# Kernel optimization log

Hardware: AMD Instinct MI355X
Metric: run time of the kernel (lower is better)

The kernel has to match this reference:

```python
import jax, jax.numpy as jnp
import numpy as np

B_, C_, T_, F_ = 1, 64, 256, 128
D_CONV, D_STATE, DT_RANK = 4, 16, 4
D_INNER = 2 * C_
EPS = 1e-5


def setup_inputs():
    key = jax.random.key(0)
    ks = jax.random.split(key, 12)
    s = 0.05
    return {
        'x': jax.random.normal(ks[0], (B_, C_, T_, F_), jnp.float32),
        'norm_w': jnp.ones((4, C_), jnp.float32),
        'in_proj_w': jax.random.normal(ks[1], (4, 2 * D_INNER, C_), jnp.float32) * s,
        'conv_w': jax.random.normal(ks[2], (4, D_INNER, 1, D_CONV), jnp.float32) * 0.3,
        'conv_b': jnp.zeros((4, D_INNER), jnp.float32),
        'x_proj_w': jax.random.normal(ks[3], (4, DT_RANK + 2 * D_STATE, D_INNER), jnp.float32) * s,
        'dt_proj_w': jax.random.normal(ks[4], (4, D_INNER, DT_RANK), jnp.float32) * 0.1,
        'dt_proj_b': jnp.log(jnp.expm1(jax.random.uniform(ks[5], (4, D_INNER), jnp.float32, 1e-3, 0.1))),
        'A_log': jnp.log(jax.random.uniform(ks[6], (4, D_INNER, D_STATE), jnp.float32, 0.5, 16.0)),
        'Dp': jnp.ones((4, D_INNER), jnp.float32),
        'out_proj_w': jax.random.normal(ks[7], (4, C_, D_INNER), jnp.float32) * s,
        'tlin_w': jax.random.normal(ks[8], (2 * C_, C_), jnp.float32) * s,
        'tlin_b': jnp.zeros((C_,), jnp.float32),
        'flin_w': jax.random.normal(ks[9], (2 * C_, C_), jnp.float32) * s,
        'flin_b': jnp.zeros((C_,), jnp.float32),
    }


def _rmsnorm(x, w):
    return x * jax.lax.rsqrt(jnp.mean(x * x, axis=-1, keepdims=True) + EPS) * w


def _mamba(u, p):
    # u: (N, L, d_model) ; selective-scan Mamba mixer
    N, L, _ = u.shape
    xz = jnp.einsum('nld,ed->nle', u, p['in_proj_w'])  # (N,L,2*di)
    x, z = jnp.split(xz, 2, axis=-1)
    # causal depthwise conv over time
    xT = jnp.swapaxes(x, 1, 2)  # (N, di, L)
    xc = jax.lax.conv_general_dilated(xT, p['conv_w'], (1,), [(D_CONV - 1, 0)],
                                      feature_group_count=D_INNER)
    x = jnp.swapaxes(jax.nn.silu(xc + p['conv_b'][None, :, None]), 1, 2)  # (N,L,di)
    xdbl = jnp.einsum('nld,ed->nle', x, p['x_proj_w'])
    dt, Bm, Cm = jnp.split(xdbl, [DT_RANK, DT_RANK + D_STATE], axis=-1)
    dt = jax.nn.softplus(jnp.einsum('nlr,dr->nld', dt, p['dt_proj_w']) + p['dt_proj_b'])
    A = -jnp.exp(p['A_log'])  # (di, ds)

    def step(h, inp):
        dt_t, B_t, C_t, x_t = inp  # (N,di),(N,ds),(N,ds),(N,di)
        dA = jnp.exp(dt_t[:, :, None] * A)  # (N,di,ds)
        h = dA * h + dt_t[:, :, None] * B_t[:, None, :] * x_t[:, :, None]
        return h, jnp.einsum('nds,ns->nd', h, C_t)

    h0 = jnp.zeros((N, D_INNER, D_STATE), u.dtype)
    _, ys = jax.lax.scan(step, h0, (jnp.swapaxes(dt, 0, 1), jnp.swapaxes(Bm, 0, 1),
                                    jnp.swapaxes(Cm, 0, 1), jnp.swapaxes(x, 0, 1)))
    y = jnp.swapaxes(ys, 0, 1) + x * p['Dp']
    y = y * jax.nn.silu(z)
    return jnp.einsum('nld,od->nlo', y, p['out_proj_w'])


def _block(u, p):
    # mamba Block with residual: out = mixer(rmsnorm(u)) + u
    return _mamba(_rmsnorm(u, p['norm_w']), p) + u


def _bimamba(u, pf, pb):
    yf = _block(u, pf)
    yb = jnp.flip(_block(jnp.flip(u, 1), pb), 1)
    return jnp.concatenate([yf, yb], axis=-1)


def _pick(i, norm_w, in_proj_w, conv_w, conv_b, x_proj_w, dt_proj_w, dt_proj_b, A_log, Dp, out_proj_w):
    return dict(norm_w=norm_w[i], in_proj_w=in_proj_w[i], conv_w=conv_w[i], conv_b=conv_b[i],
                x_proj_w=x_proj_w[i], dt_proj_w=dt_proj_w[i], dt_proj_b=dt_proj_b[i],
                A_log=A_log[i], Dp=Dp[i], out_proj_w=out_proj_w[i])


def _tfmamba(x, norm_w, in_proj_w, conv_w, conv_b, x_proj_w, dt_proj_w, dt_proj_b,
             A_log, Dp, out_proj_w, tlin_w, tlin_b, flin_w, flin_b):
    b, c, t, f = x.shape
    P = [_pick(i, norm_w, in_proj_w, conv_w, conv_b, x_proj_w, dt_proj_w, dt_proj_b, A_log, Dp, out_proj_w)
         for i in range(4)]
    # time axis
    xt = jnp.reshape(jnp.transpose(x, (0, 3, 2, 1)), (b * f, t, c))
    xt_out = _bimamba(xt, P[0], P[1])  # (b*f, t, 2c)
    xt = xt + jnp.einsum('nti,io->nto', xt_out, tlin_w) + tlin_b
    # frequency axis
    xf = jnp.reshape(jnp.transpose(jnp.reshape(xt, (b, f, t, c)), (0, 2, 1, 3)), (b * t, f, c))
    xf_out = _bimamba(xf, P[2], P[3])  # (b*t, f, 2c)
    xf = xf + jnp.einsum('nfi,io->nfo', xf_out, flin_w) + flin_b
    return jnp.transpose(jnp.reshape(xf, (b, t, f, c)), (0, 3, 1, 2))


def reference(x, norm_w, in_proj_w, conv_w, conv_b, x_proj_w, dt_proj_w, dt_proj_b,
              A_log, Dp, out_proj_w, tlin_w, tlin_b, flin_w, flin_b):
    return _tfmamba(x, norm_w, in_proj_w, conv_w, conv_b, x_proj_w, dt_proj_w, dt_proj_b,
                    A_log, Dp, out_proj_w, tlin_w, tlin_b, flin_w, flin_b)
```

## Files before the change

kernel.cpp:

```cpp
#include <hip/hip_runtime.h>
#include <math.h>

#define C_DIM 64
#define T_DIM 256
#define F_DIM 128
#define DI    128
#define DS    16
#define CK    16

typedef __attribute__((ext_vector_type(8))) short bf16x8;
typedef __attribute__((ext_vector_type(4))) float f32x4;

__device__ __forceinline__ float silu_f(float v){ return v / (1.0f + __expf(-v)); }

__device__ __forceinline__ unsigned short f2bf(float f){
  union{float f; unsigned u;} v; v.f = f;
  unsigned r = v.u + 0x7FFFu + ((v.u >> 16) & 1u);
  return (unsigned short)(r >> 16);
}

__global__ __launch_bounds__(256) void k_prep(const float* __restrict__ ipw,
                                              const float* __restrict__ opw,
                                              const float* __restrict__ xpw,
                                              const float* __restrict__ tlw,
                                              unsigned short* __restrict__ wbuf){
  const int i = blockIdx.x*256 + threadIdx.x;
  if(i < 65536){
    wbuf[i] = f2bf(ipw[i]);
  } else if(i < 98304){
    wbuf[i] = f2bf(opw[i - 65536]);
  } else if(i < 122880){
    const int j = i - 98304;
    const int p = j / 6144, rr = (j - p*6144) >> 7, k = j & 127;
    wbuf[i] = (rr < 36) ? f2bf(xpw[p*4608 + rr*128 + k]) : (unsigned short)0;
  } else {
    const int j = i - 122880;
    const int o = j >> 7, k = j & 127;
    wbuf[i] = f2bf(tlw[k*64 + o]);
  }
}

__global__ __launch_bounds__(256) void k_transpose_in(const float* __restrict__ x,
                                                      float* __restrict__ xt){
  __shared__ float tile[64][133];
  const int t = blockIdx.x;
  {
    const int fi = threadIdx.x & 127, cg = threadIdx.x >> 7;
    for(int c = cg*32; c < cg*32 + 32; ++c)
      tile[c][fi] = x[(size_t)c*32768 + (size_t)t*128 + fi];
  }
  __syncthreads();
  {
    const int ci = threadIdx.x & 63, fg = threadIdx.x >> 6;
    for(int f = fg*32; f < fg*32 + 32; ++f)
      xt[(size_t)f*16384 + (size_t)t*64 + ci] = tile[ci][f];
  }
}

__global__ __launch_bounds__(256, 2) void k_mamba(
    const float* __restrict__ src, int N, int L, long long sn, long long sl,
    int pbase,
    const float* __restrict__ norm_w,   const unsigned short* __restrict__ wbf,
    const float* __restrict__ conv_w,   const float* __restrict__ conv_b,
    const float* __restrict__ dt_proj_w,
    const float* __restrict__ dt_proj_b,const float* __restrict__ A_log,
    const float* __restrict__ Dp,       float* __restrict__ obuf)
{
  __shared__ __align__(16) unsigned short u_bf[CK][64];
  __shared__ float x_s[CK+3][132];
  __shared__ float z_s[CK][132];
  __shared__ float xc_s[CK][132];
  __shared__ __align__(16) unsigned short xc_bf[CK][128];
  __shared__ float dt_s[CK][132];
  __shared__ float dtr_s[CK][4];
  __shared__ float B_s[CK][20];
  __shared__ float C_s[CK][20];
  __shared__ __align__(16) unsigned short y_bf[CK][128];
  __shared__ float y_out[CK][68];
  __shared__ float w_cv[512];
  __shared__ float b_cv[128];
  __shared__ float w_dt[512];
  __shared__ float b_dt[128];
  __shared__ float dvec[128];
  __shared__ float nw[64];

  const int tid = threadIdx.x;
  const int bid = blockIdx.x;
  const int dir = (bid >= N) ? 1 : 0;
  const int n   = dir ? (bid - N) : bid;
  const int p   = pbase + dir;

  const int lane = tid & 63;
  const int wv   = tid >> 6;
  const int fr   = lane & 15;
  const int fk   = (lane >> 4) << 3;

  for(int i = tid; i < 512; i += 256){ w_cv[i] = conv_w[p*512 + i]; w_dt[i] = dt_proj_w[p*512 + i]; }
  if(tid < 128){ b_cv[tid] = conv_b[p*128 + tid]; b_dt[tid] = dt_proj_b[p*128 + tid]; dvec[tid] = Dp[p*128 + tid]; }
  if(tid < 64) nw[tid] = norm_w[p*64 + tid];
  for(int i = tid; i < 3*128; i += 256){ x_s[i >> 7][i & 127] = 0.0f; }

  const unsigned short* WinB  = wbf + (size_t)p*16384;
  const unsigned short* WoutB = wbf + 65536 + (size_t)p*8192;
  const unsigned short* XpB   = wbf + 98304 + (size_t)p*6144;
  bf16x8 aW[4][2];
  #pragma unroll
  for(int ot = 0; ot < 4; ++ot)
    #pragma unroll
    for(int kh = 0; kh < 2; ++kh)
      aW[ot][kh] = *(const bf16x8*)(WinB + (wv*64 + ot*16 + fr)*64 + kh*32 + fk);
  bf16x8 aO[4];
  #pragma unroll
  for(int kc = 0; kc < 4; ++kc)
    aO[kc] = *(const bf16x8*)(WoutB + (wv*16 + fr)*128 + kc*32 + fk);
  bf16x8 aXP[4];
  if(wv < 3){
    #pragma unroll
    for(int kc = 0; kc < 4; ++kc)
      aXP[kc] = *(const bf16x8*)(XpB + (wv*16 + fr)*128 + kc*32 + fk);
  }

  const int d_own = tid >> 1;
  const int sh    = (tid & 1) * 8;
  float A_r[8], h[8];
  #pragma unroll
  for(int i = 0; i < 8; ++i){
    A_r[i] = -__expf(A_log[p*2048 + d_own*16 + sh + i]) * 1.44269504f;
    h[i] = 0.0f;
  }
  __syncthreads();

  for(int c0 = 0; c0 < L; c0 += CK){
    if(c0 > 0){
      for(int i = tid; i < 3*128; i += 256){
        int r = i >> 7, ch = i & 127;
        x_s[r][ch] = x_s[CK + r][ch];
      }
    }
    {
      const int g = tid >> 4, j = tid & 15, c4 = j*4;
      const int l = c0 + g;
      const int lo = dir ? (L - 1 - l) : l;
      const float4 v = *(const float4*)(src + (size_t)n*sn + (size_t)lo*sl + c4);
      float ssq = v.x*v.x + v.y*v.y + v.z*v.z + v.w*v.w;
      ssq += __shfl_xor(ssq, 1); ssq += __shfl_xor(ssq, 2);
      ssq += __shfl_xor(ssq, 4); ssq += __shfl_xor(ssq, 8);
      const float sc = rsqrtf(ssq * (1.0f/64.0f) + 1e-5f);
      ushort4 pk;
      pk.x = f2bf(v.x * sc * nw[c4+0]);
      pk.y = f2bf(v.y * sc * nw[c4+1]);
      pk.z = f2bf(v.z * sc * nw[c4+2]);
      pk.w = f2bf(v.w * sc * nw[c4+3]);
      *(ushort4*)&u_bf[g][c4] = pk;
    }
    __syncthreads();

    {
      const bf16x8 b0 = *(const bf16x8*)&u_bf[fr][fk];
      const bf16x8 b1 = *(const bf16x8*)&u_bf[fr][32 + fk];
      #pragma unroll
      for(int ot = 0; ot < 4; ++ot){
        f32x4 acc = {0.f, 0.f, 0.f, 0.f};
        acc = __builtin_amdgcn_mfma_f32_16x16x32_bf16(aW[ot][0], b0, acc, 0, 0, 0);
        acc = __builtin_amdgcn_mfma_f32_16x16x32_bf16(aW[ot][1], b1, acc, 0, 0, 0);
        const int ob = wv*64 + ot*16 + ((lane >> 4) << 2);
        if(wv < 2){
          #pragma unroll
          for(int r = 0; r < 4; ++r) x_s[3 + fr][ob + r] = acc[r];
        } else {
          #pragma unroll
          for(int r = 0; r < 4; ++r) z_s[fr][ob + r - 128] = acc[r];
        }
      }
    }
    __syncthreads();

    {
      const int g = tid >> 4, j = tid & 15;
      #pragma unroll
      for(int i = 0; i < 8; ++i){
        const int ch = j + 16*i;
        float a = b_cv[ch];
        a += w_cv[ch*4+0] * x_s[g+0][ch];
        a += w_cv[ch*4+1] * x_s[g+1][ch];
        a += w_cv[ch*4+2] * x_s[g+2][ch];
        a += w_cv[ch*4+3] * x_s[g+3][ch];
        const float s = silu_f(a);
        xc_s[g][ch]  = s;
        xc_bf[g][ch] = f2bf(s);
      }
    }
    __syncthreads();

    if(wv < 3){
      f32x4 acc = {0.f, 0.f, 0.f, 0.f};
      #pragma unroll
      for(int kc = 0; kc < 4; ++kc){
        const bf16x8 b = *(const bf16x8*)&xc_bf[fr][kc*32 + fk];
        acc = __builtin_amdgcn_mfma_f32_16x16x32_bf16(aXP[kc], b, acc, 0, 0, 0);
      }
      const int ob36 = wv*16 + ((lane >> 4) << 2);
      #pragma unroll
      for(int r = 0; r < 4; ++r){
        const int o36 = ob36 + r;
        const float v = acc[r];
        if(o36 < 4)       dtr_s[fr][o36] = v;
        else if(o36 < 20) B_s[fr][o36 - 4] = v;
        else if(o36 < 36) C_s[fr][o36 - 20] = v;
      }
    }
    __syncthreads();

    {
      const int g = tid >> 4, j = tid & 15;
      const float r0 = dtr_s[g][0], r1 = dtr_s[g][1], r2 = dtr_s[g][2], r3 = dtr_s[g][3];
      #pragma unroll
      for(int i = 0; i < 8; ++i){
        const int d = j + 16*i;
        float a = b_dt[d] + w_dt[d*4+0]*r0 + w_dt[d*4+1]*r1 + w_dt[d*4+2]*r2 + w_dt[d*4+3]*r3;
        dt_s[g][d] = fmaxf(a, 0.0f) + log1pf(__expf(-fabsf(a)));
      }
    }
    __syncthreads();

    for(int l = 0; l < CK; ++l){
      const float dtv = dt_s[l][d_own];
      const float xv  = xc_s[l][d_own];
      const float4 b0 = *(const float4*)&B_s[l][sh];
      const float4 b1 = *(const float4*)&B_s[l][sh + 4];
      const float4 g0 = *(const float4*)&C_s[l][sh];
      const float4 g1 = *(const float4*)&C_s[l][sh + 4];
      const float bb[8] = {b0.x,b0.y,b0.z,b0.w,b1.x,b1.y,b1.z,b1.w};
      const float cc[8] = {g0.x,g0.y,g0.z,g0.w,g1.x,g1.y,g1.z,g1.w};
      const float dx = dtv * xv;
      float yp = 0.0f;
      #pragma unroll
      for(int i = 0; i < 8; ++i){
        h[i] = exp2f(dtv * A_r[i]) * h[i] + dx * bb[i];
        yp += h[i] * cc[i];
      }
      const float yo = yp + __shfl_xor(yp, 1);
      if((tid & 1) == 0) xc_s[l][d_own] = yo + xv * dvec[d_own];
    }
    __syncthreads();

    {
      const int g = tid >> 4, j = tid & 15;
      #pragma unroll
      for(int i = 0; i < 8; ++i){
        const int ch = j + 16*i;
        y_bf[g][ch] = f2bf(xc_s[g][ch] * silu_f(z_s[g][ch]));
      }
    }
    __syncthreads();

    {
      f32x4 acc = {0.f, 0.f, 0.f, 0.f};
      #pragma unroll
      for(int kc = 0; kc < 4; ++kc){
        const bf16x8 b = *(const bf16x8*)&y_bf[fr][kc*32 + fk];
        acc = __builtin_amdgcn_mfma_f32_16x16x32_bf16(aO[kc], b, acc, 0, 0, 0);
      }
      const int o2 = wv*16 + ((lane >> 4) << 2);
      #pragma unroll
      for(int r = 0; r < 4; ++r) y_out[fr][o2 + r] = acc[r];
    }
    __syncthreads();

    {
      const int o = tid & 63, lg = tid >> 6;
      #pragma unroll
      for(int li = 0; li < 4; ++li){
        const int l = c0 + lg*4 + li;
        const int lo = dir ? (L - 1 - l) : l;
        obuf[((size_t)dir*32768 + (size_t)n*L + lo)*64 + o] = y_out[lg*4 + li][o];
      }
    }
  }
}

__global__ __launch_bounds__(256) void k_comb_time(
    const float* __restrict__ xt, const float* __restrict__ obuf,
    const unsigned short* __restrict__ wbf, const float* __restrict__ tlin_b,
    float* __restrict__ xt2)
{
  __shared__ __align__(16) unsigned short in_bf[64][128];
  __shared__ float xs[64][72];
  const int tid = threadIdx.x;
  const int lane = tid & 63, wv = tid >> 6;
  const int fr = lane & 15, fk = (lane >> 4) << 3;
  const int tk0 = blockIdx.x*64;

  const unsigned short* TL = wbf + 122880;
  bf16x8 aT[4];
  #pragma unroll
  for(int kc = 0; kc < 4; ++kc)
    aT[kc] = *(const bf16x8*)(TL + (wv*16 + fr)*128 + kc*32 + fk);

  {
    const int tg = tid >> 2, q = tid & 3;
    #pragma unroll
    for(int s = 0; s < 4; ++s){
      const int c4 = q*16 + s*4;
      const float4 xv = *(const float4*)(xt   + ((size_t)tk0 + tg)*64 + c4);
      const float4 fv = *(const float4*)(obuf + ((size_t)tk0 + tg)*64 + c4);
      const float4 bv = *(const float4*)(obuf + ((size_t)32768 + tk0 + tg)*64 + c4);
      ushort4 pf, pb;
      pf.x = f2bf(fv.x + xv.x); pf.y = f2bf(fv.y + xv.y);
      pf.z = f2bf(fv.z + xv.z); pf.w = f2bf(fv.w + xv.w);
      pb.x = f2bf(bv.x + xv.x); pb.y = f2bf(bv.y + xv.y);
      pb.z = f2bf(bv.z + xv.z); pb.w = f2bf(bv.w + xv.w);
      *(ushort4*)&in_bf[tg][c4]      = pf;
      *(ushort4*)&in_bf[tg][64 + c4] = pb;
      *(float4*)&xs[tg][c4] = xv;
    }
  }
  __syncthreads();

  {
    const int ob = wv*16 + ((lane >> 4) << 2);
    const float4 tb = *(const float4*)(tlin_b + ob);
    const float tbr[4] = {tb.x, tb.y, tb.z, tb.w};
    #pragma unroll
    for(int tt = 0; tt < 4; ++tt){
      f32x4 acc = {0.f, 0.f, 0.f, 0.f};
      #pragma unroll
      for(int kc = 0; kc < 4; ++kc){
        const bf16x8 b = *(const bf16x8*)&in_bf[tt*16 + fr][kc*32 + fk];
        acc = __builtin_amdgcn_mfma_f32_16x16x32_bf16(aT[kc], b, acc, 0, 0, 0);
      }
      const int token = tt*16 + fr;
      #pragma unroll
      for(int r = 0; r < 4; ++r)
        xs[token][ob + r] += tbr[r] + acc[r];
    }
  }
  __syncthreads();

  {
    const int tg = tid >> 2, q = tid & 3;
    #pragma unroll
    for(int s = 0; s < 4; ++s){
      const int c4 = q*16 + s*4;
      *(float4*)(xt2 + ((size_t)tk0 + tg)*64 + c4) = *(const float4*)&xs[tg][c4];
    }
  }
}

__global__ __launch_bounds__(256) void k_final(
    const float* __restrict__ xt2, const float* __restrict__ obuf,
    const float* __restrict__ flin_w, const float* __restrict__ flin_b,
    float* __restrict__ out)
{
  __shared__ float res_s[128][68];
  const int t = blockIdx.x, tid = threadIdx.x;
  const int f = tid >> 1, half = tid & 1, cbase = half*32;

  const float4* xr = (const float4*)(xt2  + (size_t)f*16384 + (size_t)t*64);
  const float4* fr = (const float4*)(obuf + ((size_t)t*128 + f)*64);
  const float4* br = (const float4*)(obuf + ((size_t)32768 + (size_t)t*128 + f)*64);

  float res[32];
  {
    const float4* fb = (const float4*)(flin_b + cbase);
    #pragma unroll
    for(int q = 0; q < 8; ++q){
      const float4 xv = xr[(cbase >> 2) + q], b = fb[q];
      res[q*4+0] = xv.x + b.x; res[q*4+1] = xv.y + b.y;
      res[q*4+2] = xv.z + b.z; res[q*4+3] = xv.w + b.w;
    }
  }
  for(int i4 = 0; i4 < 16; ++i4){
    const float4 xv4 = xr[i4], of4 = fr[i4], ob4 = br[i4];
    const float af[4] = {of4.x + xv4.x, of4.y + xv4.y, of4.z + xv4.z, of4.w + xv4.w};
    const float ab[4] = {ob4.x + xv4.x, ob4.y + xv4.y, ob4.z + xv4.z, ob4.w + xv4.w};
    #pragma unroll
    for(int ii = 0; ii < 4; ++ii){
      const int i = i4*4 + ii;
      const float4* F0 = (const float4*)(flin_w + i*64 + cbase);
      const float4* F1 = (const float4*)(flin_w + (64 + i)*64 + cbase);
      #pragma unroll
      for(int q = 0; q < 8; ++q){
        const float4 w0 = F0[q], w1 = F1[q];
        res[q*4+0] += af[ii]*w0.x + ab[ii]*w1.x;
        res[q*4+1] += af[ii]*w0.y + ab[ii]*w1.y;
        res[q*4+2] += af[ii]*w0.z + ab[ii]*w1.z;
        res[q*4+3] += af[ii]*w0.w + ab[ii]*w1.w;
      }
    }
  }
  #pragma unroll
  for(int c = 0; c < 32; ++c) res_s[f][cbase + c] = res[c];
  __syncthreads();
  {
    const int fi = tid & 127, cq = tid >> 7;
    for(int c = cq*32; c < cq*32 + 32; ++c)
      out[(size_t)c*32768 + (size_t)t*128 + fi] = res_s[fi][c];
  }
}

extern "C" void kernel_launch(void* const* d_in, const int* in_sizes, int n_in,
                              void* d_out, int out_size, void* d_ws, size_t ws_size,
                              hipStream_t stream){
  (void)in_sizes; (void)n_in; (void)out_size; (void)ws_size;
  const float* x         = (const float*)d_in[0];
  const float* norm_w    = (const float*)d_in[1];
  const float* in_proj_w = (const float*)d_in[2];
  const float* conv_w    = (const float*)d_in[3];
  const float* conv_b    = (const float*)d_in[4];
  const float* x_proj_w  = (const float*)d_in[5];
  const float* dt_proj_w = (const float*)d_in[6];
  const float* dt_proj_b = (const float*)d_in[7];
  const float* A_log     = (const float*)d_in[8];
  const float* Dp        = (const float*)d_in[9];
  const float* out_proj_w= (const float*)d_in[10];
  const float* tlin_w    = (const float*)d_in[11];
  const float* tlin_b    = (const float*)d_in[12];
  const float* flin_w    = (const float*)d_in[13];
  const float* flin_b    = (const float*)d_in[14];
  float* out = (float*)d_out;

  float* xt_buf = (float*)d_ws;
  float* obuf   = xt_buf + (size_t)(1u << 21);
  float* xt2    = obuf   + (size_t)(1u << 22);

  unsigned short* wbf = (unsigned short*)d_out;

  hipLaunchKernelGGL(k_prep, dim3(512), dim3(256), 0, stream,
      in_proj_w, out_proj_w, x_proj_w, tlin_w, wbf);

  hipLaunchKernelGGL(k_transpose_in, dim3(256), dim3(256), 0, stream, x, xt_buf);

  hipLaunchKernelGGL(k_mamba, dim3(256), dim3(256), 0, stream,
      xt_buf, 128, 256, (long long)16384, (long long)64, 0,
      norm_w, wbf, conv_w, conv_b, dt_proj_w, dt_proj_b,
      A_log, Dp, obuf);

  hipLaunchKernelGGL(k_comb_time, dim3(512), dim3(256), 0, stream,
      xt_buf, obuf, wbf, tlin_b, xt2);

  hipLaunchKernelGGL(k_mamba, dim3(512), dim3(256), 0, stream,
      xt2, 256, 128, (long long)64, (long long)16384, 2,
      norm_w, wbf, conv_w, conv_b, dt_proj_w, dt_proj_b,
      A_log, Dp, obuf);

  hipLaunchKernelGGL(k_final, dim3(256), dim3(256), 0, stream,
      xt2, obuf, flin_w, flin_b, out);
}
```

Baseline: 431.3 us.

## Fuse dt softplus and gating into scan, swizzle LDS, store output directly

Result: slower. 447.6 us (+3.8%).

```diff
diff --git a/kernel.cpp b/kernel.cpp
--- a/kernel.cpp
+++ b/kernel.cpp
@@ -17,6 +17,13 @@
   union{float f; unsigned u;} v; v.f = f;
   unsigned r = v.u + 0x7FFFu + ((v.u >> 16) & 1u);
   return (unsigned short)(r >> 16);
+}
+
+__device__ __forceinline__ int swz64(int row, int col){
+  return row*64 + (col ^ ((row & 7) << 3));
+}
+__device__ __forceinline__ int swz128(int row, int col){
+  return row*128 + (col ^ ((row & 7) << 3));
 }
 
 __global__ __launch_bounds__(256) void k_prep(const float* __restrict__ ipw,
@@ -57,7 +64,7 @@
   }
 }
 
-__global__ __launch_bounds__(256, 2) void k_mamba(
+__global__ __launch_bounds__(256, 3) void k_mamba(
     const float* __restrict__ src, int N, int L, long long sn, long long sl,
     int pbase,
     const float* __restrict__ norm_w,   const unsigned short* __restrict__ wbf,
@@ -66,22 +73,17 @@
     const float* __restrict__ dt_proj_b,const float* __restrict__ A_log,
     const float* __restrict__ Dp,       float* __restrict__ obuf)
 {
-  __shared__ __align__(16) unsigned short u_bf[CK][64];
+  __shared__ __align__(16) unsigned short u_bf[CK*64];
   __shared__ float x_s[CK+3][132];
   __shared__ float z_s[CK][132];
   __shared__ float xc_s[CK][132];
-  __shared__ __align__(16) unsigned short xc_bf[CK][128];
-  __shared__ float dt_s[CK][132];
-  __shared__ float dtr_s[CK][4];
-  __shared__ float B_s[CK][20];
-  __shared__ float C_s[CK][20];
-  __shared__ __align__(16) unsigned short y_bf[CK][128];
-  __shared__ float y_out[CK][68];
+  __shared__ __align__(16) unsigned short xc_bf[CK*128];
+  __shared__ __align__(16) float dtr_s[CK][4];
+  __shared__ __align__(16) float B_s[CK][20];
+  __shared__ __align__(16) float C_s[CK][20];
+  __shared__ __align__(16) unsigned short y_bf[CK*128];
   __shared__ float w_cv[512];
   __shared__ float b_cv[128];
-  __shared__ float w_dt[512];
-  __shared__ float b_dt[128];
-  __shared__ float dvec[128];
   __shared__ float nw[64];
 
   const int tid = threadIdx.x;
@@ -95,8 +97,8 @@
   const int fr   = lane & 15;
   const int fk   = (lane >> 4) << 3;
 
-  for(int i = tid; i < 512; i += 256){ w_cv[i] = conv_w[p*512 + i]; w_dt[i] = dt_proj_w[p*512 + i]; }
-  if(tid < 128){ b_cv[tid] = conv_b[p*128 + tid]; b_dt[tid] = dt_proj_b[p*128 + tid]; dvec[tid] = Dp[p*128 + tid]; }
+  for(int i = tid; i < 512; i += 256) w_cv[i] = conv_w[p*512 + i];
+  if(tid < 128) b_cv[tid] = conv_b[p*128 + tid];
   if(tid < 64) nw[tid] = norm_w[p*64 + tid];
   for(int i = tid; i < 3*128; i += 256){ x_s[i >> 7][i & 127] = 0.0f; }
 
@@ -122,6 +124,10 @@
 
   const int d_own = tid >> 1;
   const int sh    = (tid & 1) * 8;
+  const int odd   = tid & 1;
+  const float4 wdt4  = *(const float4*)(dt_proj_w + p*512 + d_own*4);
+  const float  bdt_r = dt_proj_b[p*128 + d_own];
+  const float  dvec_r= Dp[p*128 + d_own];
   float A_r[8], h[8];
   #pragma unroll
   for(int i = 0; i < 8; ++i){
@@ -151,13 +157,13 @@
       pk.y = f2bf(v.y * sc * nw[c4+1]);
       pk.z = f2bf(v.z * sc * nw[c4+2]);
       pk.w = f2bf(v.w * sc * nw[c4+3]);
-      *(ushort4*)&u_bf[g][c4] = pk;
+      *(ushort4*)&u_bf[swz64(g, c4)] = pk;
     }
     __syncthreads();
 
     {
-      const bf16x8 b0 = *(const bf16x8*)&u_bf[fr][fk];
-      const bf16x8 b1 = *(const bf16x8*)&u_bf[fr][32 + fk];
+      const bf16x8 b0 = *(const bf16x8*)&u_bf[swz64(fr, fk)];
+      const bf16x8 b1 = *(const bf16x8*)&u_bf[swz64(fr, 32 + fk)];
       #pragma unroll
       for(int ot = 0; ot < 4; ++ot){
         f32x4 acc = {0.f, 0.f, 0.f, 0.f};
@@ -186,8 +192,8 @@
         a += w_cv[ch*4+2] * x_s[g+2][ch];
         a += w_cv[ch*4+3] * x_s[g+3][ch];
         const float s = silu_f(a);
-        xc_s[g][ch]  = s;
-        xc_bf[g][ch] = f2bf(s);
+        xc_s[g][ch] = s;
+        xc_bf[swz128(g, ch)] = f2bf(s);
       }
     }
     __syncthreads();
@@ -196,7 +202,7 @@
       f32x4 acc = {0.f, 0.f, 0.f, 0.f};
       #pragma unroll
       for(int kc = 0; kc < 4; ++kc){
-        const bf16x8 b = *(const bf16x8*)&xc_bf[fr][kc*32 + fk];
+        const bf16x8 b = *(const bf16x8*)&xc_bf[swz128(fr, kc*32 + fk)];
         acc = __builtin_amdgcn_mfma_f32_16x16x32_bf16(aXP[kc], b, acc, 0, 0, 0);
       }
       const int ob36 = wv*16 + ((lane >> 4) << 2);
@@ -212,44 +218,39 @@
     __syncthreads();
 
     {
-      const int g = tid >> 4, j = tid & 15;
-      const float r0 = dtr_s[g][0], r1 = dtr_s[g][1], r2 = dtr_s[g][2], r3 = dtr_s[g][3];
-      #pragma unroll
-      for(int i = 0; i < 8; ++i){
-        const int d = j + 16*i;
-        float a = b_dt[d] + w_dt[d*4+0]*r0 + w_dt[d*4+1]*r1 + w_dt[d*4+2]*r2 + w_dt[d*4+3]*r3;
-        dt_s[g][d] = fmaxf(a, 0.0f) + log1pf(__expf(-fabsf(a)));
-      }
-    }
-    __syncthreads();
-
-    for(int l = 0; l < CK; ++l){
-      const float dtv = dt_s[l][d_own];
-      const float xv  = xc_s[l][d_own];
-      const float4 b0 = *(const float4*)&B_s[l][sh];
-      const float4 b1 = *(const float4*)&B_s[l][sh + 4];
-      const float4 g0 = *(const float4*)&C_s[l][sh];
-      const float4 g1 = *(const float4*)&C_s[l][sh + 4];
-      const float bb[8] = {b0.x,b0.y,b0.z,b0.w,b1.x,b1.y,b1.z,b1.w};
-      const float cc[8] = {g0.x,g0.y,g0.z,g0.w,g1.x,g1.y,g1.z,g1.w};
-      const float dx = dtv * xv;
-      float yp = 0.0f;
-      #pragma unroll
-      for(int i = 0; i < 8; ++i){
-        h[i] = exp2f(dtv * A_r[i]) * h[i] + dx * bb[i];
-        yp += h[i] * cc[i];
-      }
-      const float yo = yp + __shfl_xor(yp, 1);
-      if((tid & 1) == 0) xc_s[l][d_own] = yo + xv * dvec[d_own];
-    }
-    __syncthreads();
-
-    {
-      const int g = tid >> 4, j = tid & 15;
-      #pragma unroll
-      for(int i = 0; i < 8; ++i){
-        const int ch = j + 16*i;
-        y_bf[g][ch] = f2bf(xc_s[g][ch] * silu_f(z_s[g][ch]));
+      float my_dt[8];
+      #pragma unroll
+      for(int q = 0; q < 8; ++q){
+        const int l = odd*8 + q;
+        const float4 r4 = *(const float4*)&dtr_s[l][0];
+        float a = bdt_r + wdt4.x*r4.x + wdt4.y*r4.y + wdt4.z*r4.z + wdt4.w*r4.w;
+        my_dt[q] = fmaxf(a, 0.0f) + log1pf(__expf(-fabsf(a)));
+      }
+      float ot_dt[8];
+      #pragma unroll
+      for(int q = 0; q < 8; ++q) ot_dt[q] = __shfl_xor(my_dt[q], 1);
+      #pragma unroll
+      for(int l = 0; l < CK; ++l){
+        const float dtv = ((l >> 3) == odd) ? my_dt[l & 7] : ot_dt[l & 7];
+        const float xv  = xc_s[l][d_own];
+        const float4 b0 = *(const float4*)&B_s[l][sh];
+        const float4 b1 = *(const float4*)&B_s[l][sh + 4];
+        const float4 g0 = *(const float4*)&C_s[l][sh];
+        const float4 g1 = *(const float4*)&C_s[l][sh + 4];
+        const float bb[8] = {b0.x,b0.y,b0.z,b0.w,b1.x,b1.y,b1.z,b1.w};
+        const float cc[8] = {g0.x,g0.y,g0.z,g0.w,g1.x,g1.y,g1.z,g1.w};
+        const float dx = dtv * xv;
+        float yp = 0.0f;
+        #pragma unroll
+        for(int i = 0; i < 8; ++i){
+          h[i] = exp2f(dtv * A_r[i]) * h[i] + dx * bb[i];
+          yp += h[i] * cc[i];
+        }
+        const float yo = yp + __shfl_xor(yp, 1);
+        if(odd == 0){
+          const float zv = z_s[l][d_own];
+          y_bf[swz128(l, d_own)] = f2bf((yo + xv * dvec_r) * silu_f(zv));
+        }
       }
     }
     __syncthreads();
@@ -258,23 +259,14 @@
       f32x4 acc = {0.f, 0.f, 0.f, 0.f};
       #pragma unroll
       for(int kc = 0; kc < 4; ++kc){
-        const bf16x8 b = *(const bf16x8*)&y_bf[fr][kc*32 + fk];
+        const bf16x8 b = *(const bf16x8*)&y_bf[swz128(fr, kc*32 + fk)];
         acc = __builtin_amdgcn_mfma_f32_16x16x32_bf16(aO[kc], b, acc, 0, 0, 0);
       }
       const int o2 = wv*16 + ((lane >> 4) << 2);
-      #pragma unroll
-      for(int r = 0; r < 4; ++r) y_out[fr][o2 + r] = acc[r];
-    }
-    __syncthreads();
-
-    {
-      const int o = tid & 63, lg = tid >> 6;
-      #pragma unroll
-      for(int li = 0; li < 4; ++li){
-        const int l = c0 + lg*4 + li;
-        const int lo = dir ? (L - 1 - l) : l;
-        obuf[((size_t)dir*32768 + (size_t)n*L + lo)*64 + o] = y_out[lg*4 + li][o];
-      }
+      const int l = c0 + fr;
+      const int lo = dir ? (L - 1 - l) : l;
+      float4 st; st.x = acc[0]; st.y = acc[1]; st.z = acc[2]; st.w = acc[3];
+      *(float4*)(obuf + ((size_t)dir*32768 + (size_t)n*L + lo)*64 + o2) = st;
     }
   }
 }
```
